# Performance work log

Hardware: AMD Instinct MI355X
Metric: run time of the kernel (lower is better)

## Reference

```python
import jax, jax.numpy as jnp
import numpy as np

# ---- static config (mirrors ProposalLayerModule param) ----
FEAT_STRIDE = 16
PRE_NMS_TOPN = 6000
POST_NMS_TOPN = 300
NMS_THRESH = 0.7
MIN_SIZE = 16.0
NUM_ANCHORS = 9


def _generate_anchors():
    """Replicates generate_anchors(base_size=16, ratios=[0.5,1,2], scales=[8,16,32])."""
    base = np.array([0.0, 0.0, 15.0, 15.0])
    ratios = np.array([0.5, 1.0, 2.0])
    scales = np.array([8.0, 16.0, 32.0])
    w = base[2] - base[0] + 1.0
    h = base[3] - base[1] + 1.0
    xc = base[0] + 0.5 * (w - 1.0)
    yc = base[1] + 0.5 * (h - 1.0)
    size = w * h
    ws = np.round(np.sqrt(size / ratios))
    hs = np.round(ws * ratios)
    ratio_anchors = np.stack([xc - 0.5 * (ws - 1), yc - 0.5 * (hs - 1),
                              xc + 0.5 * (ws - 1), yc + 0.5 * (hs - 1)], axis=1)
    out = []
    for a in ratio_anchors:
        aw = a[2] - a[0] + 1.0
        ah = a[3] - a[1] + 1.0
        axc = a[0] + 0.5 * (aw - 1.0)
        ayc = a[1] + 0.5 * (ah - 1.0)
        ws2 = aw * scales
        hs2 = ah * scales
        out.append(np.stack([axc - 0.5 * (ws2 - 1), ayc - 0.5 * (hs2 - 1),
                             axc + 0.5 * (ws2 - 1), ayc + 0.5 * (hs2 - 1)], axis=1))
    return np.concatenate(out, axis=0).astype(np.float32)  # (9, 4)

_ANCHORS = _generate_anchors()


def _nms_keep(iou, valid, thresh):
    """Greedy NMS over score-sorted boxes. Returns boolean keep mask."""
    n = iou.shape[0]
    idx = jnp.arange(n)
    def body(i, keep):
        sup = keep[i] & (iou[i] > thresh) & (idx > i)
        return keep & jnp.logical_not(sup)
    return jax.lax.fori_loop(0, n, body, valid)


def setup_inputs() -> dict:
    key = jax.random.key(0)
    k1, k2 = jax.random.split(key)
    H, W = 128, 192
    scores = jax.random.normal(k1, (1, 2 * NUM_ANCHORS, H, W), dtype=jnp.float32)
    # small deltas so exp(dw), exp(dh) stay in a realistic range
    bbox_deltas = jax.random.normal(k2, (1, 4 * NUM_ANCHORS, H, W), dtype=jnp.float32) * 0.1
    im_info = jnp.array([H * FEAT_STRIDE, W * FEAT_STRIDE, 1.0], dtype=jnp.float32)
    return {"scores": scores, "bbox_deltas": bbox_deltas, "im_info": im_info}


def reference(scores, bbox_deltas, im_info):
    A = NUM_ANCHORS
    s = scores[0, A:]                      # (A, H, W) fg scores
    Hf, Wf = s.shape[1], s.shape[2]
    # shifts, matching torch.meshgrid default indexing='ij' (x-major flatten)
    shift_x = jnp.arange(Wf, dtype=jnp.float32) * FEAT_STRIDE
    shift_y = jnp.arange(Hf, dtype=jnp.float32) * FEAT_STRIDE
    sx, sy = jnp.meshgrid(shift_x, shift_y, indexing='ij')   # (W, H)
    shifts = jnp.stack([sx.ravel(), sy.ravel(), sx.ravel(), sy.ravel()], axis=1)  # (K,4)
    anchors = (jnp.asarray(_ANCHORS)[None, :, :] + shifts[:, None, :]).reshape(-1, 4)  # (K*A,4)

    deltas = jnp.transpose(bbox_deltas[0], (1, 2, 0)).reshape(-1, 4)  # (H*W*A,4)
    sc = jnp.transpose(s, (1, 2, 0)).reshape(-1)                      # (H*W*A,)

    # bbox_transform_inv
    widths = anchors[:, 2] - anchors[:, 0] + 1.0
    heights = anchors[:, 3] - anchors[:, 1] + 1.0
    ctr_x = anchors[:, 0] + 0.5 * widths
    ctr_y = anchors[:, 1] + 0.5 * heights
    dx, dy, dw, dh = deltas[:, 0], deltas[:, 1], deltas[:, 2], deltas[:, 3]
    pcx = dx * widths + ctr_x
    pcy = dy * heights + ctr_y
    pw = jnp.exp(dw) * widths
    ph = jnp.exp(dh) * heights
    x1 = pcx - 0.5 * pw
    y1 = pcy - 0.5 * ph
    x2 = pcx + 0.5 * pw
    y2 = pcy + 0.5 * ph

    # clip_boxes
    x1 = jnp.clip(x1, 0.0, im_info[1] - 1.0)
    x2 = jnp.clip(x2, 0.0, im_info[1] - 1.0)
    y1 = jnp.clip(y1, 0.0, im_info[0] - 1.0)
    y2 = jnp.clip(y2, 0.0, im_info[0] - 1.0)
    boxes = jnp.stack([x1, y1, x2, y2], axis=1)

    # _filter_boxes (as a mask, jit-friendly)
    ms = MIN_SIZE * im_info[2]
    valid = ((x2 - x1 + 1.0) >= ms) & ((y2 - y1 + 1.0) >= ms)
    masked_sc = jnp.where(valid, sc, -jnp.inf)

    # sort by score descending + pre_nms_topN
    top_s, top_i = jax.lax.top_k(masked_sc, PRE_NMS_TOPN)
    b = boxes[top_i]                       # (PRE, 4), score-sorted
    vld = jnp.isfinite(top_s)

    # torchvision-style IoU (no +1) + greedy NMS
    area = (b[:, 2] - b[:, 0]) * (b[:, 3] - b[:, 1])
    ix1 = jnp.maximum(b[:, None, 0], b[None, :, 0])
    iy1 = jnp.maximum(b[:, None, 1], b[None, :, 1])
    ix2 = jnp.minimum(b[:, None, 2], b[None, :, 2])
    iy2 = jnp.minimum(b[:, None, 3], b[None, :, 3])
    inter = jnp.clip(ix2 - ix1, 0.0) * jnp.clip(iy2 - iy1, 0.0)
    iou = inter / jnp.maximum(area[:, None] + area[None, :] - inter, 1e-9)
    keep = _nms_keep(iou, vld, NMS_THRESH)

    # first post_nms_topN kept boxes (fixed-size, zero-padded), prepend batch idx 0
    cum = jnp.cumsum(keep.astype(jnp.int32))
    pos = jnp.where(keep & (cum <= POST_NMS_TOPN), cum - 1, POST_NMS_TOPN)
    rows = jnp.concatenate([jnp.zeros((PRE_NMS_TOPN, 1), jnp.float32), b], axis=1)
    out = jnp.zeros((POST_NMS_TOPN + 1, 5), jnp.float32).at[pos].set(rows)[:POST_NMS_TOPN]
    return out
```

## Files before the change

kernel.cpp:

```cpp
#include <hip/hip_runtime.h>

#define NCELL 24576
#define NTOT  221184
#define NBIN13 8192
#define TOPN  6000
#define POSTN 300
#define NPADR 6016
#define NW    94
#define CW    8
#define NCHUNK 12
#define NCB   16
#define SLOT  1024
#define CAP2  (NCB*SLOT)

__global__ void decode_kernel(const float* __restrict__ scores,
                              const float* __restrict__ deltas,
                              const float* __restrict__ iminfo,
                              float4* __restrict__ boxes,
                              unsigned* __restrict__ skeys,
                              unsigned short* __restrict__ skeys16) {
#pragma clang fp contract(off)
    int c = blockIdx.x * blockDim.x + threadIdx.x;
    if (c >= NCELL) return;
    const float AW[9] = {184.f,368.f,736.f,128.f,256.f,512.f, 88.f,176.f,352.f};
    const float AH[9] = { 96.f,192.f,384.f,128.f,256.f,512.f,176.f,352.f,704.f};
    float sx = (float)((c >> 7) << 4);
    float sy = (float)((c & 127) << 4);
    float imh = iminfo[0], imw = iminfo[1], ims = iminfo[2];
    float xhi = imw - 1.0f, yhi = imh - 1.0f;
    float ms = 16.0f * ims;
    float ctrx = sx + 8.0f, ctry = sy + 8.0f;
    const float* sbase = scores + 9 * NCELL + c;
    const float* dbase = deltas + c;
#pragma unroll
    for (int a = 0; a < 9; ++a) {
        float sc = sbase[a * NCELL];
        float dx = dbase[(4 * a + 0) * NCELL];
        float dy = dbase[(4 * a + 1) * NCELL];
        float dw = dbase[(4 * a + 2) * NCELL];
        float dh = dbase[(4 * a + 3) * NCELL];
        float pcx = dx * AW[a] + ctrx;
        float pcy = dy * AH[a] + ctry;
        float pw = expf(dw) * AW[a];
        float ph = expf(dh) * AH[a];
        float x1 = pcx - 0.5f * pw;
        float y1 = pcy - 0.5f * ph;
        float x2 = pcx + 0.5f * pw;
        float y2 = pcy + 0.5f * ph;
        x1 = fminf(fmaxf(x1, 0.0f), xhi);
        x2 = fminf(fmaxf(x2, 0.0f), xhi);
        y1 = fminf(fmaxf(y1, 0.0f), yhi);
        y2 = fminf(fmaxf(y2, 0.0f), yhi);
        bool valid = ((x2 - x1 + 1.0f) >= ms) && ((y2 - y1 + 1.0f) >= ms);
        unsigned u = __float_as_uint(sc);
        unsigned key = (u & 0x80000000u) ? ~u : (u | 0x80000000u);
        if (!valid) key = 0x007FFFFFu;
        boxes[a * NCELL + c] = make_float4(x1, y1, x2, y2);
        skeys[a * NCELL + c] = key;
        skeys16[a * NCELL + c] = (unsigned short)(key >> 16);
    }
}

__global__ __launch_bounds__(1024) void compactT_kernel(const unsigned* __restrict__ skeys,
                                                        const unsigned short* __restrict__ skeys16,
                                                        unsigned* __restrict__ meta16,
                                                        unsigned long long* __restrict__ cbuf) {
    __shared__ unsigned hist[NBIN13];
    __shared__ unsigned psum[1024];
    __shared__ unsigned csum[256];
    __shared__ unsigned sB, sAbove, sT, sCount;
    int tid = threadIdx.x, bid = blockIdx.x;
    for (int b = tid; b < NBIN13; b += 1024) hist[b] = 0u;
    if (tid == 0) sCount = 0u;
    __syncthreads();
    const uint4* s16 = (const uint4*)skeys16;
    for (int q = tid; q < NTOT / 8; q += 1024) {
        uint4 u = s16[q];
        atomicAdd(&hist[(u.x & 0xFFFFu) >> 3], 1u);
        atomicAdd(&hist[u.x >> 19], 1u);
        atomicAdd(&hist[(u.y & 0xFFFFu) >> 3], 1u);
        atomicAdd(&hist[u.y >> 19], 1u);
        atomicAdd(&hist[(u.z & 0xFFFFu) >> 3], 1u);
        atomicAdd(&hist[u.z >> 19], 1u);
        atomicAdd(&hist[(u.w & 0xFFFFu) >> 3], 1u);
        atomicAdd(&hist[u.w >> 19], 1u);
    }
    __syncthreads();
    unsigned s = 0;
#pragma unroll
    for (int q = 0; q < 8; ++q) s += hist[tid * 8 + q];
    psum[tid] = s;
    __syncthreads();
    if (tid < 256)
        csum[tid] = psum[tid * 4] + psum[tid * 4 + 1] + psum[tid * 4 + 2] + psum[tid * 4 + 3];
    __syncthreads();
    if (tid < 64) {
        int lane = tid;
        unsigned c0 = csum[lane * 4 + 0], c1 = csum[lane * 4 + 1];
        unsigned c2 = csum[lane * 4 + 2], c3 = csum[lane * 4 + 3];
        unsigned ls = c0 + c1 + c2 + c3;
        unsigned v = ls;
#pragma unroll
        for (int o = 1; o < 64; o <<= 1) {
            unsigned t = __shfl_down(v, o, 64);
            if (lane + o < 64) v += t;
        }
        unsigned sufExcl = v - ls;
        unsigned a3 = sufExcl;
        unsigned a2 = a3 + c3;
        unsigned a1 = a2 + c2;
        unsigned a0 = a1 + c1;
        if (a0 < TOPN && a0 + c0 >= TOPN) { sB = lane * 4 + 0; sAbove = a0; }
        if (a1 < TOPN && a1 + c1 >= TOPN) { sB = lane * 4 + 1; sAbove = a1; }
        if (a2 < TOPN && a2 + c2 >= TOPN) { sB = lane * 4 + 2; sAbove = a2; }
        if (a3 < TOPN && a3 + c3 >= TOPN) { sB = lane * 4 + 3; sAbove = a3; }
    }
    __syncthreads();
    if (tid < 32) {
        unsigned B = sB, above = sAbove;
        unsigned h = hist[B * 32 + tid];
        unsigned v = h;
#pragma unroll
        for (int o = 1; o < 32; o <<= 1) {
            unsigned t = __shfl_down(v, o, 64);
            if (tid + o < 32) v += t;
        }
        unsigned sufExcl = v - h;
        unsigned ab = above + sufExcl;
        if (ab < TOPN && ab + h >= TOPN) sT = B * 32 + tid;
    }
    __syncthreads();
    unsigned T = sT;
    int base = bid * (NTOT / NCB);
    const uint4* s4b = (const uint4*)(skeys + base);
    for (int q = tid; q < (NTOT / NCB) / 4; q += 1024) {
        uint4 u = s4b[q];
        unsigned k4[4] = {u.x, u.y, u.z, u.w};
#pragma unroll
        for (int k = 0; k < 4; ++k) {
            if ((k4[k] >> 19) >= T) {
                unsigned lp = atomicAdd(&sCount, 1u);
                if (lp < SLOT) {
                    int m = base + 4 * q + k;
                    unsigned n = (unsigned)((m % NCELL) * 9 + (m / NCELL));
                    cbuf[(bid << 10) + lp] =
                        ((unsigned long long)k4[k] << 32) | (unsigned long long)(~n);
                }
            }
        }
    }
    __syncthreads();
    unsigned cnt = sCount; if (cnt > SLOT) cnt = SLOT;
    for (int e = cnt + tid; e < SLOT; e += 1024) cbuf[(bid << 10) + e] = 0ULL;
    if (tid == 0) meta16[bid] = cnt;
}

__global__ __launch_bounds__(256) void rankscatter_kernel(const unsigned long long* __restrict__ cbuf,
                                                          const unsigned* __restrict__ meta16,
                                                          const float4* __restrict__ boxes,
                                                          float4* __restrict__ sortedbox) {
    __shared__ unsigned long long jk[512];
    __shared__ unsigned scnt[NCB];
    int tid = threadIdx.x;
    if (tid < NCB) scnt[tid] = meta16[tid];
    __syncthreads();
    int i = blockIdx.x * 32 + (tid >> 3);
    int slice = tid & 7;
    unsigned long long ki = cbuf[i];
    unsigned cr = 0;
    for (int jt = 0; jt < CAP2 / 512; ++jt) {
        int b = jt >> 1;
        unsigned cb = scnt[b];
        if ((jt & 1) ? (cb <= 512u) : (cb == 0u)) continue;
        __syncthreads();
        for (int q = tid; q < 512; q += 256) jk[q] = cbuf[(jt << 9) + q];
        __syncthreads();
#pragma unroll 8
        for (int j = 0; j < 64; ++j) cr += (jk[slice + (j << 3)] > ki) ? 1u : 0u;
    }
    cr += __shfl_down(cr, 4, 8);
    cr += __shfl_down(cr, 2, 8);
    cr += __shfl_down(cr, 1, 8);
    if (slice == 0 && ki != 0ULL && cr < NPADR) {
        unsigned n = ~(unsigned)ki;
        unsigned m = (n % 9u) * (unsigned)NCELL + (n / 9u);
        sortedbox[cr] = boxes[m];
    }
}

__global__ __launch_bounds__(256) void matrix_kernel(const float4* __restrict__ sortedbox,
                                                     unsigned long long* __restrict__ rowr,
                                                     unsigned long long* __restrict__ diagw,
                                                     unsigned long long* __restrict__ diagT) {
#pragma clang fp contract(off)
    __shared__ float4 jb[256];
    __shared__ float  ja[256];
    int tid = threadIdx.x;
    int lane = tid & 63, wave = tid >> 6;
    int i0 = blockIdx.y << 6;
    int i = i0 + lane;
    int w = (blockIdx.x << 2) + wave;
    int jbase = blockIdx.x << 8;
    unsigned long long word = 0ULL;

    if (jbase + 255 > i0) {
        int jg = jbase + tid;
        float4 v = (jg < NPADR) ? sortedbox[jg] : make_float4(0.f, 0.f, 0.f, 0.f);
        jb[tid] = v;
        ja[tid] = (v.z - v.x) * (v.w - v.y);
        __syncthreads();
        if (w < NW && ((w << 6) + 63) > i) {
            float4 bi = sortedbox[i];
            float ai = (bi.z - bi.x) * (bi.w - bi.y);
            int jl0 = wave << 6;
            int jg0 = (w << 6);
#pragma unroll 8
            for (int j = 0; j < 64; ++j) {
                float4 bj = jb[jl0 + j];
                float aj = ja[jl0 + j];
                float iw = fminf(bi.z, bj.z) - fmaxf(bi.x, bj.x);
                float ih = fminf(bi.w, bj.w) - fmaxf(bi.y, bj.y);
                iw = fmaxf(iw, 0.0f);
                ih = fmaxf(ih, 0.0f);
                float inter = iw * ih;
                float denom = fmaxf(ai + aj - inter, 1e-9f);
                bool sup = (jg0 + j > i) && (inter / denom > 0.7f);
                word |= (unsigned long long)sup << j;
            }
        }
    }
    if (w < NW) {
        if (w >= (i >> 6))
            rowr[(size_t)i * NW + w] = word;
        if ((i >> 9) == (w >> 3))
            diagw[((size_t)w << 9) + (i & 511)] = word;
        if (w == (i >> 6)) {
            unsigned long long col = 0ULL;
#pragma unroll
            for (int jbit = 0; jbit < 64; ++jbit) {
                unsigned long long m = __ballot((word >> jbit) & 1ULL);
                if (lane == jbit) col = m;
            }
            diagT[((size_t)w << 6) + lane] = col;
        }
    }
}

__global__ __launch_bounds__(512) void scan_kernel(const unsigned long long* __restrict__ rowr,
                                                   const unsigned long long* __restrict__ diagw,
                                                   const unsigned long long* __restrict__ diagT,
                                                   const float4* __restrict__ sortedbox,
                                                   float* __restrict__ out) {
    __shared__ __align__(16) unsigned long long cblk[2][CW * 512];
    __shared__ __align__(16) unsigned long long ldsT[2][CW * 64];
    __shared__ unsigned long long gm[128];
    __shared__ int keptArr[POSTN];
    __shared__ int s_kept, s_done;
    int tid = threadIdx.x;
    int lane = tid & 63, wave = tid >> 6;

    if (tid < 128) gm[tid] = (tid == 93) ? ~((1ULL << 48) - 1) : 0ULL;
    if (tid == 0) { s_kept = 0; s_done = 0; }
    for (int pe = tid; pe < CW * 256; pe += 512) {
        int q = pe >> 8, r = (pe & 255) << 1;
        if (q > (r >> 6))
            *(ulonglong2*)&cblk[0][(q << 9) + r] =
                *(const ulonglong2*)&diagw[((size_t)q << 9) + r];
    }
    for (int pe = tid; pe < CW * 32; pe += 512) {
        int e = pe << 1;
        *(ulonglong2*)&ldsT[0][e] = *(const ulonglong2*)&diagT[e];
    }
    __syncthreads();

    int kA = 0;
    int kB = 0;
    for (int c = 0; c < NCHUNK; ++c) {
        int buf = c & 1, nbuf = buf ^ 1;
        int wbase = c * CW;
        if (wave == 0) {
            unsigned long long dgT[CW];
#pragma unroll
            for (int q = 0; q < CW; ++q) dgT[q] = ldsT[buf][(q << 6) + lane];
            unsigned long long lowmask = (1ULL << lane) - 1ULL;
            int kept = kB;
            int done = 0;
            for (int q = 0; q < CW && wbase + q < NW; ++q) {
                int w = wbase + q;
                unsigned long long live = ~gm[w];
                if (w == NW - 1) live &= (1ULL << 48) - 1;
                if (!live) continue;
                bool alive = (live >> lane) & 1ULL;
                unsigned long long x = live;
                for (;;) {
                    bool sup = (dgT[q] & x & lowmask) != 0ULL;
                    unsigned long long xn = __ballot(alive && !sup);
                    if (xn == x) break;
                    x = xn;
                }
                unsigned long long kb = x;
                if (kb) {
                    int nk = __popcll(kb);
                    int myr = __popcll(kb & lowmask);
                    if (((kb >> lane) & 1ULL) && (kept + myr < POSTN))
                        keptArr[kept + myr] = (w << 6) + lane;
                    kept += nk;
                    if (kept >= POSTN) { kept = POSTN; done = 1; }
                }
                if (kb && !done && q < CW - 1) {
                    bool act = (lane > q) && (lane < CW);
                    int base = (lane << 9) + (q << 6);
                    unsigned long long acc = 0ULL;
                    unsigned long long t = kb;
                    while (t) {
                        int b0 = __ffsll((unsigned long long)t) - 1; t &= t - 1;
                        int b1 = 0, b2 = 0, b3 = 0, nb = 1;
                        if (t) { b1 = __ffsll((unsigned long long)t) - 1; t &= t - 1; nb = 2; }
                        if (t) { b2 = __ffsll((unsigned long long)t) - 1; t &= t - 1; nb = 3; }
                        if (t) { b3 = __ffsll((unsigned long long)t) - 1; t &= t - 1; nb = 4; }
                        unsigned long long r0 = act ? cblk[buf][base + b0] : 0ULL;
                        unsigned long long r1 = (act && nb > 1) ? cblk[buf][base + b1] : 0ULL;
                        unsigned long long r2 = (act && nb > 2) ? cblk[buf][base + b2] : 0ULL;
                        unsigned long long r3 = (act && nb > 3) ? cblk[buf][base + b3] : 0ULL;
                        acc |= (r0 | r1) | (r2 | r3);
                    }
                    if (act && acc) atomicOr(&gm[wbase + lane], acc);
                }
                if (done) break;
            }
            if (lane == 0) { s_kept = kept; s_done = done; }
        } else {
            int t = tid - 64;
            if (c + 1 < NCHUNK) {
                int wb2 = wbase + CW, rb2 = wb2 << 6;
                for (int pe = t; pe < CW * 256; pe += 448) {
                    int q = pe >> 8, r = (pe & 255) << 1;
                    if (q > (r >> 6)) {
                        ulonglong2 v = make_ulonglong2(0ULL, 0ULL);
                        if (wb2 + q < NW && rb2 + r + 1 < NPADR)
                            v = *(const ulonglong2*)&diagw[((size_t)(wb2 + q) << 9) + r];
                        *(ulonglong2*)&cblk[nbuf][(q << 9) + r] = v;
                    }
                }
                for (int pe = t; pe < CW * 32; pe += 448) {
                    int e = pe << 1, q = e >> 6;
                    ulonglong2 v = make_ulonglong2(0ULL, 0ULL);
                    if (wb2 + q < NW) v = *(const ulonglong2*)&diagT[((size_t)wb2 << 6) + e];
                    *(ulonglong2*)&ldsT[nbuf][e] = v;
                }
            }
            {
                int w2 = wbase + CW;
                int nw2 = NW - w2;
                int nr2 = kB - kA;
                if (c > 0 && nr2 > 0 && nw2 > 0) {
                    int npair = nw2 >> 1;
                    int tot = nr2 * npair;
                    for (int idx = t; idx < tot; idx += 448) {
                        int s = idx / npair, po = idx - s * npair;
                        int row = keptArr[kA + s];
                        ulonglong2 v = *(const ulonglong2*)&rowr[(size_t)row * NW + w2 + (po << 1)];
                        if (v.x) atomicOr(&gm[w2 + (po << 1)], v.x);
                        if (v.y) atomicOr(&gm[w2 + (po << 1) + 1], v.y);
                    }
                }
            }
        }
        __syncthreads();
        int keptNow = s_kept;
        bool fin = (s_done != 0) || (c == NCHUNK - 1);
        if (!fin && keptNow > kB) {
            int w1 = wbase + CW;
            int nw1 = NW - w1; if (nw1 > CW) nw1 = CW;
            int npair1 = nw1 >> 1;
            int po = tid & 3;
            for (int s = kB + (tid >> 2); s < keptNow; s += 128) {
                if (po < npair1) {
                    int row = keptArr[s];
                    ulonglong2 v = *(const ulonglong2*)&rowr[(size_t)row * NW + w1 + (po << 1)];
                    if (v.x) atomicOr(&gm[w1 + (po << 1)], v.x);
                    if (v.y) atomicOr(&gm[w1 + (po << 1) + 1], v.y);
                }
            }
        }
        kA = kB;
        kB = keptNow;
        if (fin) break;
        __syncthreads();
    }
    __syncthreads();

    int kept = s_kept;
    for (int k = tid; k < POSTN; k += 512) {
        float4 bb = make_float4(0.f, 0.f, 0.f, 0.f);
        if (k < kept) bb = sortedbox[keptArr[k]];
        out[k * 5 + 0] = 0.0f;
        out[k * 5 + 1] = bb.x;
        out[k * 5 + 2] = bb.y;
        out[k * 5 + 3] = bb.z;
        out[k * 5 + 4] = bb.w;
    }
}

extern "C" void kernel_launch(void* const* d_in, const int* in_sizes, int n_in,
                              void* d_out, int out_size, void* d_ws, size_t ws_size,
                              hipStream_t stream) {
    const float* scores = (const float*)d_in[0];
    const float* deltas = (const float*)d_in[1];
    const float* iminfo = (const float*)d_in[2];
    char* w = (char*)d_ws;
    float4*   boxes = (float4*)w;
    unsigned* skeys = (unsigned*)(w + 3538944);
    unsigned long long* rowr = (unsigned long long*)w;
    unsigned* meta16 = (unsigned*)(w + 4786176);
    unsigned long long* cbuf = (unsigned long long*)(w + 4786240);
    float4* sortedbox = (float4*)(w + 4917312);
    unsigned long long* diagw = (unsigned long long*)(w + 5013568);
    unsigned long long* diagT = (unsigned long long*)(w + 5398592);
    unsigned short* skeys16 = (unsigned short*)(w + 5446720);
    float* out = (float*)d_out;

    decode_kernel<<<NCELL / 256, 256, 0, stream>>>(scores, deltas, iminfo, boxes, skeys, skeys16);
    compactT_kernel<<<NCB, 1024, 0, stream>>>(skeys, skeys16, meta16, cbuf);
    rankscatter_kernel<<<CAP2 / 32, 256, 0, stream>>>(cbuf, meta16, boxes, sortedbox);
    matrix_kernel<<<dim3(24, 94), 256, 0, stream>>>(sortedbox, rowr, diagw, diagT);
    scan_kernel<<<1, 512, 0, stream>>>(rowr, diagw, diagT, sortedbox, out);
}
```

Baseline: 157.1 us.

## Store transposed diagonal suppression blocks and propagate intra-chunk suppression via ballots

The IoU kernel now writes the off-diagonal blocks of each chunk's diagonal band in transposed (column) form using the same ballot transpose used for diagT. The serial scan wave then reads one column word per lane from LDS and ANDs it with the kept mask. This replaces the ffs-driven loop of gathered row reads plus shared atomicOr into gm with a per-lane suppression bitmask combined through a ballot. The aim is to shorten the serial critical path of greedy NMS, at the cost of an extra 64-ballot transpose for more IoU words.

```diff
diff --git a/kernel.cpp b/kernel.cpp
--- a/kernel.cpp
+++ b/kernel.cpp
@@ -232,16 +232,17 @@
     if (w < NW) {
         if (w >= (i >> 6))
             rowr[(size_t)i * NW + w] = word;
-        if ((i >> 9) == (w >> 3))
-            diagw[((size_t)w << 9) + (i & 511)] = word;
-        if (w == (i >> 6)) {
+        if ((i >> 9) == (w >> 3) && w >= (i >> 6)) {
             unsigned long long col = 0ULL;
 #pragma unroll
             for (int jbit = 0; jbit < 64; ++jbit) {
                 unsigned long long m = __ballot((word >> jbit) & 1ULL);
                 if (lane == jbit) col = m;
             }
-            diagT[((size_t)w << 6) + lane] = col;
+            if (w == (i >> 6))
+                diagT[((size_t)w << 6) + lane] = col;
+            else
+                diagw[((size_t)w << 9) + (i & 511)] = col;
         }
     }
 }
@@ -280,15 +281,20 @@
         int wbase = c * CW;
         if (wave == 0) {
             unsigned long long dgT[CW];
+            unsigned long long gml[CW];
 #pragma unroll
             for (int q = 0; q < CW; ++q) dgT[q] = ldsT[buf][(q << 6) + lane];
+#pragma unroll
+            for (int q = 0; q < CW; ++q) gml[q] = (wbase + q < NW) ? gm[wbase + q] : ~0ULL;
             unsigned long long lowmask = (1ULL << lane) - 1ULL;
+            unsigned chunk_sup = 0;
             int kept = kB;
             int done = 0;
-            for (int q = 0; q < CW && wbase + q < NW; ++q) {
-                int w = wbase + q;
-                unsigned long long live = ~gm[w];
-                if (w == NW - 1) live &= (1ULL << 48) - 1;
+            int qmax = (NW - wbase < CW) ? (NW - wbase) : CW;
+            for (int q = 0; q < qmax; ++q) {
+                unsigned long long csup = __ballot((chunk_sup >> q) & 1u);
+                unsigned long long live = ~(gml[q] | csup);
+                if (wbase + q == NW - 1) live &= (1ULL << 48) - 1;
                 if (!live) continue;
                 bool alive = (live >> lane) & 1ULL;
                 unsigned long long x = live;
@@ -303,41 +309,30 @@
                     int nk = __popcll(kb);
                     int myr = __popcll(kb & lowmask);
                     if (((kb >> lane) & 1ULL) && (kept + myr < POSTN))
-                        keptArr[kept + myr] = (w << 6) + lane;
+                        keptArr[kept + myr] = ((wbase + q) << 6) + lane;
                     kept += nk;
-                    if (kept >= POSTN) { kept = POSTN; done = 1; }
-                }
-                if (kb && !done && q < CW - 1) {
-                    bool act = (lane > q) && (lane < CW);
-                    int base = (lane << 9) + (q << 6);
-                    unsigned long long acc = 0ULL;
-                    unsigned long long t = kb;
-                    while (t) {
-                        int b0 = __ffsll((unsigned long long)t) - 1; t &= t - 1;
-                        int b1 = 0, b2 = 0, b3 = 0, nb = 1;
-                        if (t) { b1 = __ffsll((unsigned long long)t) - 1; t &= t - 1; nb = 2; }
-                        if (t) { b2 = __ffsll((unsigned long long)t) - 1; t &= t - 1; nb = 3; }
-                        if (t) { b3 = __ffsll((unsigned long long)t) - 1; t &= t - 1; nb = 4; }
-                        unsigned long long r0 = act ? cblk[buf][base + b0] : 0ULL;
-                        unsigned long long r1 = (act && nb > 1) ? cblk[buf][base + b1] : 0ULL;
-                        unsigned long long r2 = (act && nb > 2) ? cblk[buf][base + b2] : 0ULL;
-                        unsigned long long r3 = (act && nb > 3) ? cblk[buf][base + b3] : 0ULL;
-                        acc |= (r0 | r1) | (r2 | r3);
+                    if (kept >= POSTN) { kept = POSTN; done = 1; break; }
+                    if (q < CW - 1) {
+                        unsigned long long pr[CW];
+#pragma unroll
+                        for (int t = 0; t < CW; ++t)
+                            pr[t] = cblk[buf][(t << 9) + (q << 6) + lane];
+#pragma unroll
+                        for (int t = 0; t < CW; ++t)
+                            if (t > q && (pr[t] & kb)) chunk_sup |= 1u << t;
                     }
-                    if (act && acc) atomicOr(&gm[wbase + lane], acc);
-                }
-                if (done) break;
+                }
             }
             if (lane == 0) { s_kept = kept; s_done = done; }
         } else {
             int t = tid - 64;
             if (c + 1 < NCHUNK) {
-                int wb2 = wbase + CW, rb2 = wb2 << 6;
+                int wb2 = wbase + CW;
                 for (int pe = t; pe < CW * 256; pe += 448) {
                     int q = pe >> 8, r = (pe & 255) << 1;
                     if (q > (r >> 6)) {
                         ulonglong2 v = make_ulonglong2(0ULL, 0ULL);
-                        if (wb2 + q < NW && rb2 + r + 1 < NPADR)
+                        if (wb2 + q < NW && wb2 + (r >> 6) < NW)
                             v = *(const ulonglong2*)&diagw[((size_t)(wb2 + q) << 9) + r];
                         *(ulonglong2*)&cblk[nbuf][(q << 9) + r] = v;
                     }
```

Measured after the change: 148.6 us. 5.4% less time.
